# Optimization experiments

Measured on AMD Instinct MI355X. Metric: run time of the kernel, lower is better.

Reference implementation:

```python
import jax, jax.numpy as jnp
import numpy as np

N, IN_DIM, HID, K, TOP_M = 131072, 512, 128, 256, 32


def setup_inputs() -> dict:
    key = jax.random.key(0)
    ks = jax.random.split(key, 16)
    s_in = 1.0 / np.sqrt(IN_DIM)
    s_h = 1.0 / np.sqrt(HID)
    return {
        "h0": jax.random.normal(ks[0], (N, IN_DIM), jnp.float32),
        "W1": jax.random.uniform(ks[1], (IN_DIM, HID), jnp.float32, -s_in, s_in),
        "b1": jax.random.uniform(ks[2], (HID,), jnp.float32, -s_in, s_in),
        "W2": jax.random.uniform(ks[3], (HID, HID), jnp.float32, -s_h, s_h),
        "b2": jax.random.uniform(ks[4], (HID,), jnp.float32, -s_h, s_h),
        "Wm": jax.random.uniform(ks[5], (HID, HID), jnp.float32, -s_h, s_h),
        "bm": jax.random.uniform(ks[6], (HID,), jnp.float32, -s_h, s_h),
        "Wt": jax.random.uniform(ks[7], (HID, HID), jnp.float32, -s_h, s_h),
        "bt": jax.random.uniform(ks[8], (HID,), jnp.float32, -s_h, s_h),
        "Wp": jax.random.uniform(ks[9], (HID, HID), jnp.float32, -s_h, s_h),
        "bp": jax.random.uniform(ks[10], (HID,), jnp.float32, -s_h, s_h),
        "cb_m": jax.random.normal(ks[11], (K, HID), jnp.float32),
        "cb_t": jax.random.normal(ks[12], (K, HID), jnp.float32),
        "cb_p": jax.random.normal(ks[13], (K, HID), jnp.float32),
        "ws": jax.random.uniform(ks[14], (HID,), jnp.float32, -s_h, s_h),
        "wb": jax.random.uniform(ks[15], (1,), jnp.float32, -s_h, s_h),
    }


def _l2n(x):
    return x / jnp.clip(jnp.linalg.norm(x, axis=-1, keepdims=True), 1e-12, None)


def _cos_dist(z, cb):
    # cosine-sim VQ codebook 'distance': [N, K] similarity matrix
    return jnp.einsum("nd,kd->nk", _l2n(z), _l2n(cb))


def reference(h0, W1, b1, W2, b2, Wm, bm, Wt, bt, Wp, bp, cb_m, cb_t, cb_p, ws, wb):
    # encoder MLP
    H = jax.nn.relu(jax.nn.relu(h0 @ W1 + b1) @ W2 + b2)  # [N, HID]
    dist_m = _cos_dist(H @ Wm + bm, cb_m)  # [N, K]
    dist_t = _cos_dist(H @ Wt + bt, cb_t)
    dist_p = _cos_dist(H @ Wp + bp, cb_p)
    # default path: argmin over codebook axis
    k_m = jnp.argmin(dist_m, axis=-1)
    k_t = jnp.argmin(dist_t, axis=-1)
    k_p = jnp.argmin(dist_p, axis=-1)
    codes = jnp.stack([k_m, k_t, k_p], axis=-1)  # [N, 3]
    alpha = jax.nn.sigmoid(H @ ws + wb[0])  # [N]
    n = codes.shape[0]
    M = min(TOP_M, n)
    _, key_idx = jax.lax.top_k(alpha, M)
    key_idx = jnp.clip(key_idx, 0, n - 1)
    return codes, key_idx, codes[key_idx]
```

## Files before the change

kernel.cpp:

```cpp
#include <hip/hip_runtime.h>

#define NROWS   131072
#define INDIM   512
#define HIDD    128
#define KCB     256
#define RPB     128

#define OFF_A     0u
#define OFF_CV    98304u
#define OFF_LOG   99072u
#define OFF_HIST  230144u
#define OFF_META  295680u
#define OFF_LISTA 295696u
#define OFF_LISTB 295824u
#define LISTB_CAP 2048u

__device__ __forceinline__ unsigned order_key(float f) {
    unsigned u = __float_as_uint(f);
    return u ^ ((u & 0x80000000u) ? 0xFFFFFFFFu : 0x80000000u);
}

__global__ __launch_bounds__(256) void vq_precompute(
    const float* __restrict__ Wm, const float* __restrict__ bm,
    const float* __restrict__ Wt, const float* __restrict__ bt,
    const float* __restrict__ Wp, const float* __restrict__ bp,
    const float* __restrict__ cbm, const float* __restrict__ cbt, const float* __restrict__ cbp,
    float* __restrict__ A, float* __restrict__ cv, unsigned* __restrict__ hist)
{
    for (unsigned i = blockIdx.x * 256u + threadIdx.x; i < 65536u + 16u; i += 24u * 256u)
        hist[i] = 0u;

    const int c  = blockIdx.x >> 3;
    const int jg = (blockIdx.x & 7) * 16;
    const float* W  = (c == 0) ? Wm  : (c == 1) ? Wt  : Wp;
    const float* bb = (c == 0) ? bm  : (c == 1) ? bt  : bp;
    const float* cb = (c == 0) ? cbm : (c == 1) ? cbt : cbp;
    const int k = threadIdx.x;
    const float4* cbr = (const float4*)(cb + (size_t)k * HIDD);
    float s = 0.f;
    for (int d = 0; d < HIDD / 4; ++d) {
        float4 x = cbr[d];
        s += x.x * x.x + x.y * x.y + x.z * x.z + x.w * x.w;
    }
    const float rn = 1.f / fmaxf(sqrtf(s), 1e-12f);
    for (int j = jg; j < jg + 16; ++j) {
        const float4* wr = (const float4*)(W + (size_t)j * HIDD);
        float acc = 0.f;
        for (int d = 0; d < HIDD / 4; ++d) {
            float4 x = cbr[d]; float4 w = wr[d];
            acc += x.x * w.x + x.y * w.y + x.z * w.z + x.w * w.w;
        }
        A[((size_t)c * HIDD + j) * KCB + k] = acc * rn;
    }
    if (jg == 0) {
        const float4* br = (const float4*)bb;
        float acc = 0.f;
        for (int d = 0; d < HIDD / 4; ++d) {
            float4 x = cbr[d]; float4 w = br[d];
            acc += x.x * w.x + x.y * w.y + x.z * w.z + x.w * w.w;
        }
        cv[(size_t)c * KCB + k] = acc * rn;
    }
}

__global__ __launch_bounds__(256) void vq_main(
    const float* __restrict__ h0, const float* __restrict__ W1, const float* __restrict__ bias1,
    const float* __restrict__ W2, const float* __restrict__ bias2,
    const float* __restrict__ Amat, const float* __restrict__ cv, const float* __restrict__ wsv,
    int* __restrict__ codes, float* __restrict__ logits, unsigned* __restrict__ hist)
{
    __shared__ float T[HIDD * RPB];
    __shared__ float S[4096];

    const int t  = threadIdx.x;
    const int tx = t & 15;
    const int ty = t >> 4;
    const int row0 = blockIdx.x * RPB;

    {
        float acc[8][8] = {};
        const int srow = t >> 1;
        const int sq   = (t & 1) * 8;
        const float* hp = h0 + (size_t)(row0 + srow) * INDIM + sq;
        float4 ha = *(const float4*)(hp);
        float4 hb = *(const float4*)(hp + 4);
        for (int kc = 0; kc < INDIM; kc += 16) {
            float* Sb = S + ((kc >> 4) & 1) * 2048;
            Sb[(sq + 0) * RPB + srow] = ha.x;
            Sb[(sq + 1) * RPB + srow] = ha.y;
            Sb[(sq + 2) * RPB + srow] = ha.z;
            Sb[(sq + 3) * RPB + srow] = ha.w;
            Sb[(sq + 4) * RPB + srow] = hb.x;
            Sb[(sq + 5) * RPB + srow] = hb.y;
            Sb[(sq + 6) * RPB + srow] = hb.z;
            Sb[(sq + 7) * RPB + srow] = hb.w;
            __syncthreads();
            if (kc + 16 < INDIM) {
                ha = *(const float4*)(hp + kc + 16);
                hb = *(const float4*)(hp + kc + 20);
            }
            const float* Wb = W1 + (size_t)kc * HIDD + 4 * tx;
            #pragma unroll 4
            for (int k = 0; k < 16; ++k) {
                float4 a0 = *(const float4*)&Sb[k * RPB + 8 * ty];
                float4 a1 = *(const float4*)&Sb[k * RPB + 8 * ty + 4];
                float4 b0 = *(const float4*)(Wb + k * HIDD);
                float4 b1 = *(const float4*)(Wb + k * HIDD + 64);
                float aa[8] = {a0.x, a0.y, a0.z, a0.w, a1.x, a1.y, a1.z, a1.w};
                float bb[8] = {b0.x, b0.y, b0.z, b0.w, b1.x, b1.y, b1.z, b1.w};
                #pragma unroll
                for (int r = 0; r < 8; ++r)
                    #pragma unroll
                    for (int j = 0; j < 8; ++j)
                        acc[r][j] = fmaf(aa[r], bb[j], acc[r][j]);
            }
        }
        float4 bv0 = *(const float4*)&bias1[4 * tx];
        float4 bv1 = *(const float4*)&bias1[4 * tx + 64];
        float ba[8] = {bv0.x, bv0.y, bv0.z, bv0.w, bv1.x, bv1.y, bv1.z, bv1.w};
        #pragma unroll
        for (int i = 0; i < 2; ++i)
            #pragma unroll
            for (int j = 0; j < 4; ++j) {
                const int c = 4 * tx + 64 * i + j;
                float4 lo, hi;
                lo.x = fmaxf(acc[0][i * 4 + j] + ba[i * 4 + j], 0.f);
                lo.y = fmaxf(acc[1][i * 4 + j] + ba[i * 4 + j], 0.f);
                lo.z = fmaxf(acc[2][i * 4 + j] + ba[i * 4 + j], 0.f);
                lo.w = fmaxf(acc[3][i * 4 + j] + ba[i * 4 + j], 0.f);
                hi.x = fmaxf(acc[4][i * 4 + j] + ba[i * 4 + j], 0.f);
                hi.y = fmaxf(acc[5][i * 4 + j] + ba[i * 4 + j], 0.f);
                hi.z = fmaxf(acc[6][i * 4 + j] + ba[i * 4 + j], 0.f);
                hi.w = fmaxf(acc[7][i * 4 + j] + ba[i * 4 + j], 0.f);
                *(float4*)&T[c * RPB + 8 * ty]     = lo;
                *(float4*)&T[c * RPB + 8 * ty + 4] = hi;
            }
    }
    __syncthreads();

    {
        float acc[8][8] = {};
        const float* Wb = W2 + 4 * tx;
        #pragma unroll 4
        for (int k = 0; k < HIDD; ++k) {
            float4 a0 = *(const float4*)&T[k * RPB + 8 * ty];
            float4 a1 = *(const float4*)&T[k * RPB + 8 * ty + 4];
            float4 b0 = *(const float4*)(Wb + k * HIDD);
            float4 b1 = *(const float4*)(Wb + k * HIDD + 64);
            float aa[8] = {a0.x, a0.y, a0.z, a0.w, a1.x, a1.y, a1.z, a1.w};
            float bb[8] = {b0.x, b0.y, b0.z, b0.w, b1.x, b1.y, b1.z, b1.w};
            #pragma unroll
            for (int r = 0; r < 8; ++r)
                #pragma unroll
                for (int j = 0; j < 8; ++j)
                    acc[r][j] = fmaf(aa[r], bb[j], acc[r][j]);
        }
        __syncthreads();
        float4 bv0 = *(const float4*)&bias2[4 * tx];
        float4 bv1 = *(const float4*)&bias2[4 * tx + 64];
        float ba[8] = {bv0.x, bv0.y, bv0.z, bv0.w, bv1.x, bv1.y, bv1.z, bv1.w};
        #pragma unroll
        for (int i = 0; i < 2; ++i)
            #pragma unroll
            for (int j = 0; j < 4; ++j) {
                const int c = 4 * tx + 64 * i + j;
                float4 lo, hi;
                lo.x = fmaxf(acc[0][i * 4 + j] + ba[i * 4 + j], 0.f);
                lo.y = fmaxf(acc[1][i * 4 + j] + ba[i * 4 + j], 0.f);
                lo.z = fmaxf(acc[2][i * 4 + j] + ba[i * 4 + j], 0.f);
                lo.w = fmaxf(acc[3][i * 4 + j] + ba[i * 4 + j], 0.f);
                hi.x = fmaxf(acc[4][i * 4 + j] + ba[i * 4 + j], 0.f);
                hi.y = fmaxf(acc[5][i * 4 + j] + ba[i * 4 + j], 0.f);
                hi.z = fmaxf(acc[6][i * 4 + j] + ba[i * 4 + j], 0.f);
                hi.w = fmaxf(acc[7][i * 4 + j] + ba[i * 4 + j], 0.f);
                *(float4*)&T[c * RPB + 8 * ty]     = lo;
                *(float4*)&T[c * RPB + 8 * ty + 4] = hi;
            }
    }
    __syncthreads();
    if (t < HIDD) S[t] = wsv[t];

    for (int cbk = 0; cbk < 3; ++cbk) {
        float mv[8] = {3.4e38f, 3.4e38f, 3.4e38f, 3.4e38f, 3.4e38f, 3.4e38f, 3.4e38f, 3.4e38f};
        int   mi[8] = {0, 0, 0, 0, 0, 0, 0, 0};
        #pragma unroll 1
        for (int half = 0; half < 2; ++half) {
            float acc[8][8] = {};
            const float* Ab = Amat + (size_t)cbk * HIDD * KCB + 128 * half + 4 * tx;
            #pragma unroll 4
            for (int k = 0; k < HIDD; ++k) {
                float4 a0 = *(const float4*)&T[k * RPB + 8 * ty];
                float4 a1 = *(const float4*)&T[k * RPB + 8 * ty + 4];
                float4 b0 = *(const float4*)(Ab + (size_t)k * KCB);
                float4 b1 = *(const float4*)(Ab + (size_t)k * KCB + 64);
                float aa[8] = {a0.x, a0.y, a0.z, a0.w, a1.x, a1.y, a1.z, a1.w};
                float bb[8] = {b0.x, b0.y, b0.z, b0.w, b1.x, b1.y, b1.z, b1.w};
                #pragma unroll
                for (int r = 0; r < 8; ++r)
                    #pragma unroll
                    for (int j = 0; j < 8; ++j)
                        acc[r][j] = fmaf(aa[r], bb[j], acc[r][j]);
            }
            const float* cvb = cv + cbk * KCB + 128 * half + 4 * tx;
            float4 c0 = *(const float4*)cvb;
            float4 c1 = *(const float4*)(cvb + 64);
            float ca[8] = {c0.x, c0.y, c0.z, c0.w, c1.x, c1.y, c1.z, c1.w};
            #pragma unroll
            for (int i = 0; i < 2; ++i)
                #pragma unroll
                for (int j = 0; j < 4; ++j) {
                    const int c = 128 * half + 64 * i + 4 * tx + j;
                    #pragma unroll
                    for (int r = 0; r < 8; ++r) {
                        float v = acc[r][4 * i + j] + ca[4 * i + j];
                        if (v < mv[r]) { mv[r] = v; mi[r] = c; }
                    }
                }
        }
        #pragma unroll
        for (int d = 1; d < 16; d <<= 1) {
            #pragma unroll
            for (int r = 0; r < 8; ++r) {
                float ov = __shfl_xor(mv[r], d);
                int   oi = __shfl_xor(mi[r], d);
                if (ov < mv[r] || (ov == mv[r] && oi < mi[r])) { mv[r] = ov; mi[r] = oi; }
            }
        }
        if (tx == 0) {
            #pragma unroll
            for (int r = 0; r < 8; ++r)
                codes[(size_t)(row0 + 8 * ty + r) * 3 + cbk] = mi[r];
        }
    }

    __syncthreads();
    if (t < RPB) {
        float s = 0.f;
        #pragma unroll 8
        for (int k = 0; k < HIDD; ++k) s = fmaf(T[k * RPB + t], S[k], s);
        logits[row0 + t] = s;
        atomicAdd(&hist[order_key(s) >> 16], 1u);
    }
}

__global__ __launch_bounds__(1024) void vq_findp(const unsigned* __restrict__ hist,
                                                 unsigned* __restrict__ meta)
{
    __shared__ unsigned Tb[1024];
    __shared__ unsigned sIg, sPg;
    const int t = threadIdx.x;
    unsigned s = 0;
    const uint4* hv = (const uint4*)(hist + (size_t)t * 64);
    for (int j = 0; j < 16; ++j) { uint4 h = hv[j]; s += h.x + h.y + h.z + h.w; }
    Tb[t] = s;
    __syncthreads();
    for (int d = 1; d < 1024; d <<= 1) {
        unsigned v = (t + d < 1024) ? Tb[t + d] : 0u;
        __syncthreads();
        Tb[t] += v;
        __syncthreads();
    }
    const unsigned Ti = Tb[t];
    const unsigned P  = Ti - s;
    if (P < 32u && Ti >= 32u) { sIg = (unsigned)t; sPg = P; }
    __syncthreads();
    const int ig = (int)sIg;
    const unsigned Pg = sPg;
    if (t < 64) {
        unsigned c = hist[ig * 64 + t];
        unsigned Tw = c;
        #pragma unroll
        for (int d = 1; d < 64; d <<= 1) {
            unsigned v = __shfl_down(Tw, d);
            if (t + d < 64) Tw += v;
        }
        unsigned Pl = Pg + Tw - c;
        if (Pl < 32u && Pl + c >= 32u) { meta[2] = (unsigned)(ig * 64 + t); meta[3] = Pl; }
    }
}

__global__ __launch_bounds__(256) void vq_collect(
    const float* __restrict__ logits, unsigned* __restrict__ meta,
    unsigned* __restrict__ listA, unsigned* __restrict__ listB)
{
    const int i = blockIdx.x * 256 + threadIdx.x;
    const unsigned key = order_key(logits[i]);
    const unsigned p = meta[2];
    const unsigned b = key >> 16;
    if (b > p) {
        unsigned idx = atomicAdd(&meta[0], 1u);
        if (idx < 64u) { listA[2 * idx] = key; listA[2 * idx + 1] = (unsigned)i; }
    } else if (b == p) {
        unsigned idx = atomicAdd(&meta[1], 1u);
        if (idx < LISTB_CAP) { listB[2 * idx] = key; listB[2 * idx + 1] = (unsigned)i; }
    }
}

__global__ __launch_bounds__(256) void vq_final(
    const unsigned* __restrict__ meta,
    const unsigned* __restrict__ listA, const unsigned* __restrict__ listB,
    const int* __restrict__ codes,
    int* __restrict__ outki, int* __restrict__ outsel)
{
    __shared__ unsigned Ks[64 + LISTB_CAP];
    __shared__ unsigned Is[64 + LISTB_CAP];
    __shared__ int sel[32];
    const int t = threadIdx.x;
    const unsigned nAv = meta[0];
    const unsigned nBv = meta[1];
    const int nA = (nAv > 64u) ? 64 : (int)nAv;
    const int nB = (nBv > LISTB_CAP) ? (int)LISTB_CAP : (int)nBv;
    const int n  = nA + nB;
    for (int j = t; j < n; j += 256) {
        if (j < nA) { Ks[j] = listA[2 * j]; Is[j] = listA[2 * j + 1]; }
        else        { int jj = j - nA; Ks[j] = listB[2 * jj]; Is[j] = listB[2 * jj + 1]; }
    }
    __syncthreads();
    for (int j = t; j < n; j += 256) {
        const unsigned kj = Ks[j], ij = Is[j];
        int rank = 0;
        for (int m = 0; m < n; ++m) {
            const unsigned km = Ks[m], im = Is[m];
            rank += (km > kj) || (km == kj && im < ij);
        }
        if (rank < 32) sel[rank] = (int)ij;
    }
    __syncthreads();
    if (t < 32) outki[t] = sel[t];
    if (t < 96) outsel[t] = codes[3 * sel[t / 3] + (t % 3)];
}

extern "C" void kernel_launch(void* const* d_in, const int* in_sizes, int n_in,
                              void* d_out, int out_size, void* d_ws, size_t ws_size,
                              hipStream_t stream)
{
    (void)in_sizes; (void)n_in; (void)out_size; (void)ws_size;

    const float* h0  = (const float*)d_in[0];
    const float* W1  = (const float*)d_in[1];
    const float* b1  = (const float*)d_in[2];
    const float* W2  = (const float*)d_in[3];
    const float* b2  = (const float*)d_in[4];
    const float* Wm  = (const float*)d_in[5];
    const float* bm  = (const float*)d_in[6];
    const float* Wt  = (const float*)d_in[7];
    const float* bt  = (const float*)d_in[8];
    const float* Wp  = (const float*)d_in[9];
    const float* bp  = (const float*)d_in[10];
    const float* cbm = (const float*)d_in[11];
    const float* cbt = (const float*)d_in[12];
    const float* cbp = (const float*)d_in[13];
    const float* wsv = (const float*)d_in[14];

    float*    wsf   = (float*)d_ws;
    unsigned* wsu   = (unsigned*)d_ws;
    float*    A     = wsf + OFF_A;
    float*    cvv   = wsf + OFF_CV;
    float*    logit = wsf + OFF_LOG;
    unsigned* hist  = wsu + OFF_HIST;
    unsigned* meta  = wsu + OFF_META;
    unsigned* listA = wsu + OFF_LISTA;
    unsigned* listB = wsu + OFF_LISTB;

    int* codes  = (int*)d_out;
    int* outki  = codes + (size_t)NROWS * 3;
    int* outsel = outki + 32;

    vq_precompute<<<24, 256, 0, stream>>>(Wm, bm, Wt, bt, Wp, bp, cbm, cbt, cbp, A, cvv, hist);
    vq_main<<<NROWS / RPB, 256, 0, stream>>>(h0, W1, b1, W2, b2, A, cvv, wsv, codes, logit, hist);
    vq_findp<<<1, 1024, 0, stream>>>(hist, meta);
    vq_collect<<<NROWS / 256, 256, 0, stream>>>(logit, meta, listA, listB);
    vq_final<<<1, 256, 0, stream>>>(meta, listA, listB, codes, outki, outsel);
}
```

Before: 739.5 us.

## Double threads per block with 4x8 micro-tiles and XOR-swizzled LDS activations

The main fused kernel now runs 512 threads per block instead of 256. Each thread computes a 4-row by 8-column micro-tile instead of 8x8 in every GEMM stage: the encoder layers and the three codebook projections. This cuts accumulator registers per thread, aiming for more resident waves and better latency hiding. The shared activation tile T is also XOR-swizzled by column group to reduce LDS bank conflicts. In exchange, each FMA has less register reuse, and every thread loads the weight/codebook float4s from global memory twice as often relative to its work.

```diff
diff --git a/kernel.cpp b/kernel.cpp
--- a/kernel.cpp
+++ b/kernel.cpp
@@ -5,6 +5,7 @@
 #define HIDD    128
 #define KCB     256
 #define RPB     128
+#define THREADS 512
 
 #define OFF_A     0u
 #define OFF_CV    98304u
@@ -14,6 +15,8 @@
 #define OFF_LISTA 295696u
 #define OFF_LISTB 295824u
 #define LISTB_CAP 2048u
+
+#define TIDX(c, r) ((c) * RPB + ((r) ^ ((((c) >> 2) & 7) << 2)))
 
 __device__ __forceinline__ unsigned order_key(float f) {
     unsigned u = __float_as_uint(f);
@@ -63,7 +66,7 @@
     }
 }
 
-__global__ __launch_bounds__(256) void vq_main(
+__global__ __launch_bounds__(THREADS) void vq_main(
     const float* __restrict__ h0, const float* __restrict__ W1, const float* __restrict__ bias1,
     const float* __restrict__ W2, const float* __restrict__ bias2,
     const float* __restrict__ Amat, const float* __restrict__ cv, const float* __restrict__ wsv,
@@ -78,38 +81,30 @@
     const int row0 = blockIdx.x * RPB;
 
     {
-        float acc[8][8] = {};
-        const int srow = t >> 1;
-        const int sq   = (t & 1) * 8;
+        float acc[4][8] = {};
+        const int srow = t >> 2;
+        const int sq   = (t & 3) * 4;
         const float* hp = h0 + (size_t)(row0 + srow) * INDIM + sq;
-        float4 ha = *(const float4*)(hp);
-        float4 hb = *(const float4*)(hp + 4);
+        float4 ha = *(const float4*)hp;
         for (int kc = 0; kc < INDIM; kc += 16) {
             float* Sb = S + ((kc >> 4) & 1) * 2048;
             Sb[(sq + 0) * RPB + srow] = ha.x;
             Sb[(sq + 1) * RPB + srow] = ha.y;
             Sb[(sq + 2) * RPB + srow] = ha.z;
             Sb[(sq + 3) * RPB + srow] = ha.w;
-            Sb[(sq + 4) * RPB + srow] = hb.x;
-            Sb[(sq + 5) * RPB + srow] = hb.y;
-            Sb[(sq + 6) * RPB + srow] = hb.z;
-            Sb[(sq + 7) * RPB + srow] = hb.w;
             __syncthreads();
-            if (kc + 16 < INDIM) {
+            if (kc + 16 < INDIM)
                 ha = *(const float4*)(hp + kc + 16);
-                hb = *(const float4*)(hp + kc + 20);
-            }
             const float* Wb = W1 + (size_t)kc * HIDD + 4 * tx;
             #pragma unroll 4
             for (int k = 0; k < 16; ++k) {
-                float4 a0 = *(const float4*)&Sb[k * RPB + 8 * ty];
-                float4 a1 = *(const float4*)&Sb[k * RPB + 8 * ty + 4];
+                float4 a0 = *(const float4*)&Sb[k * RPB + 4 * ty];
                 float4 b0 = *(const float4*)(Wb + k * HIDD);
                 float4 b1 = *(const float4*)(Wb + k * HIDD + 64);
-                float aa[8] = {a0.x, a0.y, a0.z, a0.w, a1.x, a1.y, a1.z, a1.w};
+                float aa[4] = {a0.x, a0.y, a0.z, a0.w};
                 float bb[8] = {b0.x, b0.y, b0.z, b0.w, b1.x, b1.y, b1.z, b1.w};
                 #pragma unroll
-                for (int r = 0; r < 8; ++r)
+                for (int r = 0; r < 4; ++r)
                     #pragma unroll
                     for (int j = 0; j < 8; ++j)
                         acc[r][j] = fmaf(aa[r], bb[j], acc[r][j]);
@@ -123,34 +118,28 @@
             #pragma unroll
             for (int j = 0; j < 4; ++j) {
                 const int c = 4 * tx + 64 * i + j;
-                float4 lo, hi;
-                lo.x = fmaxf(acc[0][i * 4 + j] + ba[i * 4 + j], 0.f);
-                lo.y = fmaxf(acc[1][i * 4 + j] + ba[i * 4 + j], 0.f);
-                lo.z = fmaxf(acc[2][i * 4 + j] + ba[i * 4 + j], 0.f);
-                lo.w = fmaxf(acc[3][i * 4 + j] + ba[i * 4 + j], 0.f);
-                hi.x = fmaxf(acc[4][i * 4 + j] + ba[i * 4 + j], 0.f);
-                hi.y = fmaxf(acc[5][i * 4 + j] + ba[i * 4 + j], 0.f);
-                hi.z = fmaxf(acc[6][i * 4 + j] + ba[i * 4 + j], 0.f);
-                hi.w = fmaxf(acc[7][i * 4 + j] + ba[i * 4 + j], 0.f);
-                *(float4*)&T[c * RPB + 8 * ty]     = lo;
-                *(float4*)&T[c * RPB + 8 * ty + 4] = hi;
+                float4 v;
+                v.x = fmaxf(acc[0][i * 4 + j] + ba[i * 4 + j], 0.f);
+                v.y = fmaxf(acc[1][i * 4 + j] + ba[i * 4 + j], 0.f);
+                v.z = fmaxf(acc[2][i * 4 + j] + ba[i * 4 + j], 0.f);
+                v.w = fmaxf(acc[3][i * 4 + j] + ba[i * 4 + j], 0.f);
+                *(float4*)&T[TIDX(c, 4 * ty)] = v;
             }
     }
     __syncthreads();
 
     {
-        float acc[8][8] = {};
+        float acc[4][8] = {};
         const float* Wb = W2 + 4 * tx;
         #pragma unroll 4
         for (int k = 0; k < HIDD; ++k) {
-            float4 a0 = *(const float4*)&T[k * RPB + 8 * ty];
-            float4 a1 = *(const float4*)&T[k * RPB + 8 * ty + 4];
+            float4 a0 = *(const float4*)&T[TIDX(k, 4 * ty)];
             float4 b0 = *(const float4*)(Wb + k * HIDD);
             float4 b1 = *(const float4*)(Wb + k * HIDD + 64);
-            float aa[8] = {a0.x, a0.y, a0.z, a0.w, a1.x, a1.y, a1.z, a1.w};
+            float aa[4] = {a0.x, a0.y, a0.z, a0.w};
             float bb[8] = {b0.x, b0.y, b0.z, b0.w, b1.x, b1.y, b1.z, b1.w};
             #pragma unroll
-            for (int r = 0; r < 8; ++r)
+            for (int r = 0; r < 4; ++r)
                 #pragma unroll
                 for (int j = 0; j < 8; ++j)
                     acc[r][j] = fmaf(aa[r], bb[j], acc[r][j]);
@@ -164,39 +153,33 @@
             #pragma unroll
             for (int j = 0; j < 4; ++j) {
                 const int c = 4 * tx + 64 * i + j;
-                float4 lo, hi;
-                lo.x = fmaxf(acc[0][i * 4 + j] + ba[i * 4 + j], 0.f);
-                lo.y = fmaxf(acc[1][i * 4 + j] + ba[i * 4 + j], 0.f);
-                lo.z = fmaxf(acc[2][i * 4 + j] + ba[i * 4 + j], 0.f);
-                lo.w = fmaxf(acc[3][i * 4 + j] + ba[i * 4 + j], 0.f);
-                hi.x = fmaxf(acc[4][i * 4 + j] + ba[i * 4 + j], 0.f);
-                hi.y = fmaxf(acc[5][i * 4 + j] + ba[i * 4 + j], 0.f);
-                hi.z = fmaxf(acc[6][i * 4 + j] + ba[i * 4 + j], 0.f);
-                hi.w = fmaxf(acc[7][i * 4 + j] + ba[i * 4 + j], 0.f);
-                *(float4*)&T[c * RPB + 8 * ty]     = lo;
-                *(float4*)&T[c * RPB + 8 * ty + 4] = hi;
+                float4 v;
+                v.x = fmaxf(acc[0][i * 4 + j] + ba[i * 4 + j], 0.f);
+                v.y = fmaxf(acc[1][i * 4 + j] + ba[i * 4 + j], 0.f);
+                v.z = fmaxf(acc[2][i * 4 + j] + ba[i * 4 + j], 0.f);
+                v.w = fmaxf(acc[3][i * 4 + j] + ba[i * 4 + j], 0.f);
+                *(float4*)&T[TIDX(c, 4 * ty)] = v;
             }
     }
     __syncthreads();
     if (t < HIDD) S[t] = wsv[t];
 
     for (int cbk = 0; cbk < 3; ++cbk) {
-        float mv[8] = {3.4e38f, 3.4e38f, 3.4e38f, 3.4e38f, 3.4e38f, 3.4e38f, 3.4e38f, 3.4e38f};
-        int   mi[8] = {0, 0, 0, 0, 0, 0, 0, 0};
+        float mv[4] = {3.4e38f, 3.4e38f, 3.4e38f, 3.4e38f};
+        int   mi[4] = {0, 0, 0, 0};
         #pragma unroll 1
         for (int half = 0; half < 2; ++half) {
-            float acc[8][8] = {};
+            float acc[4][8] = {};
             const float* Ab = Amat + (size_t)cbk * HIDD * KCB + 128 * half + 4 * tx;
             #pragma unroll 4
             for (int k = 0; k < HIDD; ++k) {
-                float4 a0 = *(const float4*)&T[k * RPB + 8 * ty];
-                float4 a1 = *(const float4*)&T[k * RPB + 8 * ty + 4];
+                float4 a0 = *(const float4*)&T[TIDX(k, 4 * ty)];
                 float4 b0 = *(const float4*)(Ab + (size_t)k * KCB);
                 float4 b1 = *(const float4*)(Ab + (size_t)k * KCB + 64);
-                float aa[8] = {a0.x, a0.y, a0.z, a0.w, a1.x, a1.y, a1.z, a1.w};
+                float aa[4] = {a0.x, a0.y, a0.z, a0.w};
                 float bb[8] = {b0.x, b0.y, b0.z, b0.w, b1.x, b1.y, b1.z, b1.w};
                 #pragma unroll
-                for (int r = 0; r < 8; ++r)
+                for (int r = 0; r < 4; ++r)
                     #pragma unroll
                     for (int j = 0; j < 8; ++j)
                         acc[r][j] = fmaf(aa[r], bb[j], acc[r][j]);
@@ -211,7 +194,7 @@
                 for (int j = 0; j < 4; ++j) {
                     const int c = 128 * half + 64 * i + 4 * tx + j;
                     #pragma unroll
-                    for (int r = 0; r < 8; ++r) {
+                    for (int r = 0; r < 4; ++r) {
                         float v = acc[r][4 * i + j] + ca[4 * i + j];
                         if (v < mv[r]) { mv[r] = v; mi[r] = c; }
                     }
@@ -220,7 +203,7 @@
         #pragma unroll
         for (int d = 1; d < 16; d <<= 1) {
             #pragma unroll
-            for (int r = 0; r < 8; ++r) {
+            for (int r = 0; r < 4; ++r) {
                 float ov = __shfl_xor(mv[r], d);
                 int   oi = __shfl_xor(mi[r], d);
                 if (ov < mv[r] || (ov == mv[r] && oi < mi[r])) { mv[r] = ov; mi[r] = oi; }
@@ -228,8 +211,8 @@
         }
         if (tx == 0) {
             #pragma unroll
-            for (int r = 0; r < 8; ++r)
-                codes[(size_t)(row0 + 8 * ty + r) * 3 + cbk] = mi[r];
+            for (int r = 0; r < 4; ++r)
+                codes[(size_t)(row0 + 4 * ty + r) * 3 + cbk] = mi[r];
         }
     }
 
@@ -237,7 +220,7 @@
     if (t < RPB) {
         float s = 0.f;
         #pragma unroll 8
-        for (int k = 0; k < HIDD; ++k) s = fmaf(T[k * RPB + t], S[k], s);
+        for (int k = 0; k < HIDD; ++k) s = fmaf(T[TIDX(k, t)], S[k], s);
         logits[row0 + t] = s;
         atomicAdd(&hist[order_key(s) >> 16], 1u);
     }
@@ -367,7 +350,7 @@
     int* outsel = outki + 32;
 
     vq_precompute<<<24, 256, 0, stream>>>(Wm, bm, Wt, bt, Wp, bp, cbm, cbt, cbp, A, cvv, hist);
-    vq_main<<<NROWS / RPB, 256, 0, stream>>>(h0, W1, b1, W2, b2, A, cvv, wsv, codes, logit, hist);
+    vq_main<<<NROWS / RPB, THREADS, 0, stream>>>(h0, W1, b1, W2, b2, A, cvv, wsv, codes, logit, hist);
     vq_findp<<<1, 1024, 0, stream>>>(hist, meta);
     vq_collect<<<NROWS / 256, 256, 0, stream>>>(logit, meta, listA, listB);
     vq_final<<<1, 256, 0, stream>>>(meta, listA, listB, codes, outki, outsel);
```

After: 1.101 ms. +48.9%, slower.
